# Kernel optimization log

Hardware: AMD Instinct MI355X
Metric: run time of the kernel (lower is better)

The kernel has to match this reference:

```python
import jax, jax.numpy as jnp
import numpy as np

D = 1024      # n_embd
H = 16        # n_head
DH = D // H   # head dim = 64
FF = 4 * D    # 4096
EPS = 1e-5
MASKED_BIAS = -10000.0


def gelu_new(x):
    # GPT-2 'gelu_new': 0.5*x*(1+tanh(sqrt(2/pi)*(x+0.044715*x^3)))
    c = np.sqrt(2.0 / np.pi).astype(np.float32)
    return 0.5 * x * (1.0 + jnp.tanh(c * (x + 0.044715 * x * x * x)))


def layer_norm(x, g, b):
    mu = jnp.mean(x, axis=-1, keepdims=True)
    var = jnp.mean(jnp.square(x - mu), axis=-1, keepdims=True)
    return (x - mu) * jax.lax.rsqrt(var + EPS) * g + b


def setup_inputs() -> dict:
    key = jax.random.key(0)
    ks = jax.random.split(key, 8)
    B, S = 4, 2048
    std = 0.02
    return {
        "hidden_states": jax.random.normal(ks[0], (B, S, D), jnp.float32),
        "ln1_g": jnp.ones((D,), jnp.float32),
        "ln1_b": jnp.zeros((D,), jnp.float32),
        "w_attn": std * jax.random.normal(ks[1], (D, 3 * D), jnp.float32),
        "b_attn": jnp.zeros((3 * D,), jnp.float32),
        "w_attn_proj": std * jax.random.normal(ks[2], (D, D), jnp.float32),
        "b_attn_proj": jnp.zeros((D,), jnp.float32),
        "ln2_g": jnp.ones((D,), jnp.float32),
        "ln2_b": jnp.zeros((D,), jnp.float32),
        "w_fc": std * jax.random.normal(ks[3], (D, FF), jnp.float32),
        "b_fc": jnp.zeros((FF,), jnp.float32),
        "w_mlp_proj": std * jax.random.normal(ks[4], (FF, D), jnp.float32),
        "b_mlp_proj": jnp.zeros((D,), jnp.float32),
    }


def reference(hidden_states, ln1_g, ln1_b, w_attn, b_attn, w_attn_proj, b_attn_proj,
              ln2_g, ln2_b, w_fc, b_fc, w_mlp_proj, b_mlp_proj):
    B, S, _ = hidden_states.shape

    # --- self-attention ---
    x = layer_norm(hidden_states, ln1_g, ln1_b)
    qkv = x @ w_attn + b_attn                       # [B,S,3D]
    q, k, v = jnp.split(qkv, 3, axis=-1)
    # split heads -> [B,H,S,DH]
    q = q.reshape(B, S, H, DH).transpose(0, 2, 1, 3)
    k = k.reshape(B, S, H, DH).transpose(0, 2, 1, 3)
    v = v.reshape(B, S, H, DH).transpose(0, 2, 1, 3)

    w = jnp.einsum('bhqd,bhkd->bhqk', q, k) / jnp.sqrt(jnp.float32(DH))
    causal = jnp.tril(jnp.ones((S, S), bool))       # [S,S]
    w = jnp.where(causal, w, jnp.float32(MASKED_BIAS))
    w = jax.nn.softmax(w, axis=-1)
    a = jnp.einsum('bhqk,bhkd->bhqd', w, v)         # [B,H,S,DH]
    a = a.transpose(0, 2, 1, 3).reshape(B, S, D)
    a = a @ w_attn_proj + b_attn_proj
    hidden_states = hidden_states + a

    # --- MLP ---
    m = layer_norm(hidden_states, ln2_g, ln2_b)
    m = gelu_new(m @ w_fc + b_fc) @ w_mlp_proj + b_mlp_proj
    return hidden_states + m
```

## Files before the change

### kernel.cpp

```cpp
#include <hip/hip_runtime.h>
#include <hip/hip_bf16.h>
#include <cstddef>

#define SEQ   2048
#define DMODEL 1024
#define NHEAD 16
#define HDIM  64
#define FFDIM 4096
#define QT    (SEQ / 64)

typedef __attribute__((ext_vector_type(8))) short bf16x8;
typedef __attribute__((ext_vector_type(4))) short bf16x4;
typedef __attribute__((ext_vector_type(4))) float f32x4;

__device__ __forceinline__ unsigned short f2b(float x) {
  __hip_bfloat16 h = __float2bfloat16(x);
  return __builtin_bit_cast(unsigned short, h);
}
__device__ __forceinline__ float b2f(short u) {
  unsigned x = ((unsigned)(unsigned short)u) << 16;
  return __builtin_bit_cast(float, x);
}
__device__ __forceinline__ void gl16(const short* g, short* l) {
  __builtin_amdgcn_global_load_lds(
      (const __attribute__((address_space(1))) void*)g,
      (__attribute__((address_space(3))) void*)l, 16, 0, 0);
}

__global__ __launch_bounds__(256)
void ln_kernel(const float* __restrict__ x, const float* __restrict__ g,
               const float* __restrict__ b, short* __restrict__ y) {
  const int row = blockIdx.x;
  const int t = threadIdx.x;
  const float* xr = x + (size_t)row * DMODEL;
  float4 v = *(const float4*)(xr + t * 4);
  float s = v.x + v.y + v.z + v.w;
  float q = v.x * v.x + v.y * v.y + v.z * v.z + v.w * v.w;
  #pragma unroll
  for (int off = 32; off; off >>= 1) {
    s += __shfl_xor(s, off);
    q += __shfl_xor(q, off);
  }
  __shared__ float ss[4], qq[4];
  if ((t & 63) == 0) { ss[t >> 6] = s; qq[t >> 6] = q; }
  __syncthreads();
  s = ss[0] + ss[1] + ss[2] + ss[3];
  q = qq[0] + qq[1] + qq[2] + qq[3];
  const float mean = s * (1.f / DMODEL);
  const float var = q * (1.f / DMODEL) - mean * mean;
  const float rstd = rsqrtf(var + 1e-5f);
  float4 gv = *(const float4*)(g + t * 4);
  float4 bv = *(const float4*)(b + t * 4);
  bf16x4 o;
  o[0] = (short)f2b((v.x - mean) * rstd * gv.x + bv.x);
  o[1] = (short)f2b((v.y - mean) * rstd * gv.y + bv.y);
  o[2] = (short)f2b((v.z - mean) * rstd * gv.z + bv.z);
  o[3] = (short)f2b((v.w - mean) * rstd * gv.w + bv.w);
  *(bf16x4*)(y + (size_t)row * DMODEL + t * 4) = o;
}

__device__ __forceinline__ float gelu_new_f(float x) {
  const float c = 0.7978845608028654f;
  float u = c * (x + 0.044715f * x * x * x);
  float e = __expf(2.f * u);
  float t = 1.f - 2.f / (e + 1.f);
  return 0.5f * x * (1.f + t);
}

__global__ __launch_bounds__(256)
void wconv4_kernel(const float* __restrict__ w0, short* __restrict__ t0,
                   const float* __restrict__ w1, short* __restrict__ t1,
                   const float* __restrict__ w2, short* __restrict__ t2,
                   const float* __restrict__ w3, short* __restrict__ t3) {
  int id = blockIdx.x;
  const float* W; short* Wt; int K, N;
  if (id < 768)       { W = w0; Wt = t0; K = 1024; N = 3072; }
  else if (id < 1024) { id -= 768;  W = w1; Wt = t1; K = 1024; N = 1024; }
  else if (id < 2048) { id -= 1024; W = w2; Wt = t2; K = 1024; N = 4096; }
  else                { id -= 2048; W = w3; Wt = t3; K = 4096; N = 1024; }
  const int nt = N >> 6;
  const int n0 = (id % nt) * 64, k0 = (id / nt) * 64;
  const int t = threadIdx.x;
  __shared__ short tile[64][72];
  #pragma unroll
  for (int i = 0; i < 4; ++i) {
    const int row = i * 16 + (t >> 4);
    const int col4 = (t & 15) * 4;
    float4 v = *(const float4*)(W + (size_t)(k0 + row) * N + n0 + col4);
    tile[col4 + 0][row] = (short)f2b(v.x);
    tile[col4 + 1][row] = (short)f2b(v.y);
    tile[col4 + 2][row] = (short)f2b(v.z);
    tile[col4 + 3][row] = (short)f2b(v.w);
  }
  __syncthreads();
  #pragma unroll
  for (int i = 0; i < 2; ++i) {
    const int cc = t + i * 256;
    const int nr = cc >> 3, k8 = (cc & 7) * 8;
    bf16x8 vv;
    #pragma unroll
    for (int j = 0; j < 8; ++j) vv[j] = tile[nr][k8 + j];
    *(bf16x8*)(Wt + (size_t)(n0 + nr) * K + k0 + k8) = vv;
  }
}

template <bool OUTBF, bool GELU, bool RES>
__global__ __launch_bounds__(256)
void gemm_bf16(const short* __restrict__ A, const short* __restrict__ Bt,
               const float* __restrict__ bias, const float* __restrict__ R,
               void* __restrict__ C, int M, int N, int K) {
  __shared__ short As[128 * 64];
  __shared__ short Bs[128 * 64];
  const int t = threadIdx.x, lane = t & 63, w = t >> 6;
  const int g = lane >> 4, la = lane & 15;
  const int bn = blockIdx.x, bm = blockIdx.y;
  const int wm = w >> 1, wn = w & 1;

  const int srow = t >> 3;
  const int scolb = ((t & 7) * 16) ^ ((srow & 7) << 4);
  const short* Ag = A + (size_t)(bm * 128 + srow) * K + (scolb >> 1);
  const short* Bg = Bt + (size_t)(bn * 128 + srow) * K + (scolb >> 1);
  short* Asl = As + t * 8;
  short* Bsl = Bs + t * 8;

  f32x4 acc[4][4];
  #pragma unroll
  for (int i = 0; i < 4; ++i)
    #pragma unroll
    for (int j = 0; j < 4; ++j) acc[i][j] = (f32x4){0.f, 0.f, 0.f, 0.f};

  const int KT = K >> 6;
  for (int kt = 0; kt < KT; ++kt) {
    __syncthreads();
    #pragma unroll
    for (int i = 0; i < 4; ++i) {
      gl16(Ag + (size_t)i * 32 * K + kt * 64, Asl + i * 2048);
      gl16(Bg + (size_t)i * 32 * K + kt * 64, Bsl + i * 2048);
    }
    __syncthreads();
    #pragma unroll
    for (int ks = 0; ks < 2; ++ks) {
      bf16x8 af[4], bfr[4];
      #pragma unroll
      for (int mi = 0; mi < 4; ++mi) {
        const int row = wm * 64 + mi * 16 + la;
        af[mi] = *(const bf16x8*)((const char*)As + row * 128 +
                                  ((ks * 64 + g * 16) ^ ((row & 7) << 4)));
      }
      #pragma unroll
      for (int ni = 0; ni < 4; ++ni) {
        const int row = wn * 64 + ni * 16 + la;
        bfr[ni] = *(const bf16x8*)((const char*)Bs + row * 128 +
                                   ((ks * 64 + g * 16) ^ ((row & 7) << 4)));
      }
      #pragma unroll
      for (int mi = 0; mi < 4; ++mi)
        #pragma unroll
        for (int ni = 0; ni < 4; ++ni)
          acc[mi][ni] = __builtin_amdgcn_mfma_f32_16x16x32_bf16(
              af[mi], bfr[ni], acc[mi][ni], 0, 0, 0);
    }
  }

  const int crow0 = bm * 128 + wm * 64 + g * 4;
  const int ccol0 = bn * 128 + wn * 64 + la;
  float bl[4];
  #pragma unroll
  for (int ni = 0; ni < 4; ++ni) bl[ni] = bias[ccol0 + ni * 16];
  #pragma unroll
  for (int mi = 0; mi < 4; ++mi) {
    #pragma unroll
    for (int r = 0; r < 4; ++r) {
      const size_t row = (size_t)(crow0 + mi * 16 + r);
      #pragma unroll
      for (int ni = 0; ni < 4; ++ni) {
        float v = acc[mi][ni][r] + bl[ni];
        if (GELU) v = gelu_new_f(v);
        if (RES) v += R[row * N + ccol0 + ni * 16];
        if (OUTBF)
          ((short*)C)[row * N + ccol0 + ni * 16] = (short)f2b(v);
        else
          ((float*)C)[row * N + ccol0 + ni * 16] = v;
      }
    }
  }
}

__global__ __launch_bounds__(256)
void prep_kernel(const short* __restrict__ qkv, short* __restrict__ Qb,
                 short* __restrict__ Kb, short* __restrict__ Vtb) {
  const int st = blockIdx.x, h = blockIdx.y, b = blockIdx.z;
  const int t = threadIdx.x;
  const int s0 = st * 64;
  const size_t bh = (size_t)b * NHEAD + h;
  const float qscale = 0.125f * 1.44269504088896f;
  __shared__ short vt[64][72];
  #pragma unroll
  for (int i = 0; i < 2; ++i) {
    const int cc = t + i * 256;
    const int r = cc >> 3, d8 = (cc & 7) * 8;
    const short* src = qkv + ((size_t)b * SEQ + s0 + r) * 3072 + h * 64 + d8;
    bf16x8 q8 = *(const bf16x8*)(src);
    #pragma unroll
    for (int j = 0; j < 8; ++j) q8[j] = (short)f2b(b2f(q8[j]) * qscale);
    *(bf16x8*)(Qb + (bh * SEQ + s0 + r) * 64 + d8) = q8;
    bf16x8 k8 = *(const bf16x8*)(src + 1024);
    *(bf16x8*)(Kb + (bh * SEQ + s0 + r) * 64 + d8) = k8;
    bf16x8 v8 = *(const bf16x8*)(src + 2048);
    #pragma unroll
    for (int j = 0; j < 8; ++j) vt[d8 + j][r] = v8[j];
  }
  __syncthreads();
  #pragma unroll
  for (int i = 0; i < 2; ++i) {
    const int cc = t + i * 256;
    const int d = cc >> 3, s8 = (cc & 7) * 8;
    bf16x8 vv;
    #pragma unroll
    for (int j = 0; j < 8; ++j) vv[j] = vt[d][s8 + j];
    *(bf16x8*)(Vtb + (bh * 64 + d) * SEQ + s0 + s8) = vv;
  }
}

__global__ __launch_bounds__(256)
void mha_kernel(const short* __restrict__ Qb, const short* __restrict__ Kb,
                const short* __restrict__ Vtb, short* __restrict__ out) {
  const int p = blockIdx.x, h = blockIdx.y, b = blockIdx.z;
  const int t = threadIdx.x, lane = t & 63, w = t >> 6;
  const int g = lane >> 4, la = lane & 15;
  const size_t bh = (size_t)b * NHEAD + h;

  __shared__ short Ks[64 * 64];
  __shared__ short Vts[64 * 64];
  __shared__ short Ps[4][16 * 64];

  const int srow = t >> 3;
  const int scolb = ((t & 7) * 16) ^ ((srow & 7) << 4);

  #pragma unroll 1
  for (int e = 0; e < 2; ++e) {
    const int qt = e ? (QT - 1 - p) : p;

    const short* qrow = Qb + (bh * SEQ + (size_t)qt * 64 + w * 16 + la) * 64;
    const bf16x8 qf0 = *(const bf16x8*)(qrow + g * 8);
    const bf16x8 qf1 = *(const bf16x8*)(qrow + 32 + g * 8);

    float o[16];
    #pragma unroll
    for (int i = 0; i < 16; ++i) o[i] = 0.f;
    float m = -1e30f, l = 0.f;

    for (int kt = 0; kt <= qt; ++kt) {
      const int k0 = kt * 64;
      __syncthreads();
      #pragma unroll
      for (int i = 0; i < 2; ++i) {
        const int r = srow + i * 32;
        gl16(Kb + (bh * SEQ + k0 + r) * 64 + (scolb >> 1), Ks + i * 2048 + t * 8);
        gl16(Vtb + (bh * 64 + r) * SEQ + k0 + (scolb >> 1), Vts + i * 2048 + t * 8);
      }
      __syncthreads();

      float sv[16];
      #pragma unroll
      for (int mt = 0; mt < 4; ++mt) {
        const int ar = mt * 16 + la;
        const int ab = ar * 128 + ((g * 16) ^ ((ar & 7) << 4));
        bf16x8 ka0 = *(const bf16x8*)((char*)Ks + ab);
        bf16x8 ka1 = *(const bf16x8*)((char*)Ks + (ab ^ 64));
        f32x4 sa = {0.f, 0.f, 0.f, 0.f};
        sa = __builtin_amdgcn_mfma_f32_16x16x32_bf16(ka0, qf0, sa, 0, 0, 0);
        sa = __builtin_amdgcn_mfma_f32_16x16x32_bf16(ka1, qf1, sa, 0, 0, 0);
        sv[mt * 4 + 0] = sa[0]; sv[mt * 4 + 1] = sa[1];
        sv[mt * 4 + 2] = sa[2]; sv[mt * 4 + 3] = sa[3];
      }

      if (kt == qt) {
        const int qrel = w * 16 + la;
        #pragma unroll
        for (int idx = 0; idx < 16; ++idx) {
          const int krel = (idx >> 2) * 16 + g * 4 + (idx & 3);
          if (krel > qrel) sv[idx] = -14426.950408889634f;
        }
      }

      float t8[8], t4[4], t2[2];
      #pragma unroll
      for (int i = 0; i < 8; ++i) t8[i] = fmaxf(sv[2 * i], sv[2 * i + 1]);
      #pragma unroll
      for (int i = 0; i < 4; ++i) t4[i] = fmaxf(t8[2 * i], t8[2 * i + 1]);
      t2[0] = fmaxf(t4[0], t4[1]); t2[1] = fmaxf(t4[2], t4[3]);
      float tmax = fmaxf(t2[0], t2[1]);
      tmax = fmaxf(tmax, __shfl_xor(tmax, 16));
      tmax = fmaxf(tmax, __shfl_xor(tmax, 32));

      const bool skip = __all(tmax <= m + 11.5f) != 0;
      const float mn = skip ? m : fmaxf(m, tmax);

      float ss8[8], ss4[4];
      #pragma unroll
      for (int i = 0; i < 16; ++i) sv[i] = exp2f(sv[i] - mn);
      #pragma unroll
      for (int i = 0; i < 8; ++i) ss8[i] = sv[2 * i] + sv[2 * i + 1];
      #pragma unroll
      for (int i = 0; i < 4; ++i) ss4[i] = ss8[2 * i] + ss8[2 * i + 1];
      float ps = (ss4[0] + ss4[1]) + (ss4[2] + ss4[3]);
      ps += __shfl_xor(ps, 16);
      ps += __shfl_xor(ps, 32);

      if (skip) {
        l += ps;
      } else {
        const float sc = exp2f(m - mn);
        l = l * sc + ps;
        m = mn;
        #pragma unroll
        for (int r = 0; r < 4; ++r) {
          const float scr = __shfl(sc, (g << 2) + r);
          o[r] *= scr; o[4 + r] *= scr; o[8 + r] *= scr; o[12 + r] *= scr;
        }
      }

      #pragma unroll
      for (int mt = 0; mt < 4; ++mt) {
        #pragma unroll
        for (int r2 = 0; r2 < 2; ++r2) {
          const unsigned pk = (unsigned)f2b(sv[mt * 4 + r2 * 2]) |
                              ((unsigned)f2b(sv[mt * 4 + r2 * 2 + 1]) << 16);
          const int kk = mt * 16 + g * 4 + r2 * 2;
          const int pb = la * 128 + ((kk * 2) ^ ((la & 7) << 4));
          *(unsigned*)((char*)Ps[w] + pb) = pk;
        }
      }
      asm volatile("s_waitcnt lgkmcnt(0)" ::: "memory");
      __builtin_amdgcn_sched_barrier(0);

      const int pb0 = la * 128 + ((g * 16) ^ ((la & 7) << 4));
      const bf16x8 pa0 = *(const bf16x8*)((char*)Ps[w] + pb0);
      const bf16x8 pa1 = *(const bf16x8*)((char*)Ps[w] + (pb0 ^ 64));
      #pragma unroll
      for (int nt = 0; nt < 4; ++nt) {
        const int dr = nt * 16 + la;
        const int vb = dr * 128 + ((g * 16) ^ ((dr & 7) << 4));
        bf16x8 vb0 = *(const bf16x8*)((char*)Vts + vb);
        bf16x8 vb1 = *(const bf16x8*)((char*)Vts + (vb ^ 64));
        f32x4 oa = {o[nt * 4 + 0], o[nt * 4 + 1], o[nt * 4 + 2], o[nt * 4 + 3]};
        oa = __builtin_amdgcn_mfma_f32_16x16x32_bf16(pa0, vb0, oa, 0, 0, 0);
        oa = __builtin_amdgcn_mfma_f32_16x16x32_bf16(pa1, vb1, oa, 0, 0, 0);
        o[nt * 4 + 0] = oa[0]; o[nt * 4 + 1] = oa[1];
        o[nt * 4 + 2] = oa[2]; o[nt * 4 + 3] = oa[3];
      }
    }

    const float linv = 1.f / l;
    #pragma unroll
    for (int r = 0; r < 4; ++r) {
      const float li = __shfl(linv, (g << 2) + r);
      const int qrow_g = qt * 64 + w * 16 + g * 4 + r;
      #pragma unroll
      for (int nt = 0; nt < 4; ++nt) {
        out[((size_t)b * SEQ + qrow_g) * DMODEL + h * 64 + nt * 16 + la] =
            (short)f2b(o[nt * 4 + r] * li);
      }
    }
  }
}

extern "C" void kernel_launch(void* const* d_in, const int* in_sizes, int n_in,
                              void* d_out, int out_size, void* d_ws, size_t ws_size,
                              hipStream_t stream) {
  const float* hidden      = (const float*)d_in[0];
  const float* ln1_g       = (const float*)d_in[1];
  const float* ln1_b       = (const float*)d_in[2];
  const float* w_attn      = (const float*)d_in[3];
  const float* b_attn      = (const float*)d_in[4];
  const float* w_attn_proj = (const float*)d_in[5];
  const float* b_attn_proj = (const float*)d_in[6];
  const float* ln2_g       = (const float*)d_in[7];
  const float* ln2_b       = (const float*)d_in[8];
  const float* w_fc        = (const float*)d_in[9];
  const float* b_fc        = (const float*)d_in[10];
  const float* w_mlp_proj  = (const float*)d_in[11];
  const float* b_mlp_proj  = (const float*)d_in[12];
  float* out = (float*)d_out;

  const int Bn = in_sizes[0] / (SEQ * DMODEL);
  const int M = Bn * SEQ;

  char* W = (char*)d_ws;
  const size_t szMD2 = (size_t)M * DMODEL * 2;
  short* xln_b  = (short*)W;
  short* qkv_b  = (short*)(W + szMD2);
  short* a1_b   = qkv_b;
  char*  p2     = W + szMD2 + (size_t)M * FFDIM * 2;
  short* Qb     = (short*)p2;
  short* Kb     = Qb + (size_t)M * DMODEL;
  short* Vtb    = Kb + (size_t)M * DMODEL;
  short* attn_b = Vtb + (size_t)M * DMODEL;
  float* h2     = (float*)(p2 + 4 * szMD2);
  short* wat    = (short*)(p2 + 4 * szMD2 + (size_t)M * DMODEL * 4);
  short* wpt    = wat + (size_t)3 * DMODEL * DMODEL;
  short* wft    = wpt + (size_t)DMODEL * DMODEL;
  short* wmt    = wft + (size_t)FFDIM * DMODEL;

  wconv4_kernel<<<3072, 256, 0, stream>>>(w_attn, wat, w_attn_proj, wpt,
                                          w_fc, wft, w_mlp_proj, wmt);
  ln_kernel<<<M, 256, 0, stream>>>(hidden, ln1_g, ln1_b, xln_b);
  gemm_bf16<true, false, false><<<dim3(3 * DMODEL / 128, M / 128), 256, 0, stream>>>(
      xln_b, wat, b_attn, nullptr, qkv_b, M, 3 * DMODEL, DMODEL);
  prep_kernel<<<dim3(SEQ / 64, NHEAD, Bn), 256, 0, stream>>>(qkv_b, Qb, Kb, Vtb);
  mha_kernel<<<dim3(QT / 2, NHEAD, Bn), 256, 0, stream>>>(Qb, Kb, Vtb, attn_b);
  gemm_bf16<false, false, true><<<dim3(DMODEL / 128, M / 128), 256, 0, stream>>>(
      attn_b, wpt, b_attn_proj, hidden, h2, M, DMODEL, DMODEL);
  ln_kernel<<<M, 256, 0, stream>>>(h2, ln2_g, ln2_b, xln_b);
  gemm_bf16<true, true, false><<<dim3(FFDIM / 128, M / 128), 256, 0, stream>>>(
      xln_b, wft, b_fc, nullptr, a1_b, M, FFDIM, DMODEL);
  gemm_bf16<false, false, true><<<dim3(DMODEL / 128, M / 128), 256, 0, stream>>>(
      a1_b, wmt, b_mlp_proj, h2, out, M, DMODEL, FFDIM);
}
```

Before: 565.3 us.

## Fuse QKV head-split into GEMM epilogue and double-buffer attention K/V tiles

Folds the softmax query scale into the converted QKV weights and bias, and has the QKV GEMM epilogue scatter Q, K and V straight into per-head layouts. This leaves the prep kernel only the V transpose, cutting a full read and write of the QKV buffer. The attention kernel now runs both query tiles in one flattened loop with double-buffered K/V LDS tiles, prefetching the next tile while computing the current one, and raises wave priority around the MFMA sections. The scattered epilogue stores are less coalesced, and the extra LDS buffers may lower occupancy.

```diff
diff --git a/kernel.cpp b/kernel.cpp
--- a/kernel.cpp
+++ b/kernel.cpp
@@ -12,6 +12,8 @@
 typedef __attribute__((ext_vector_type(8))) short bf16x8;
 typedef __attribute__((ext_vector_type(4))) short bf16x4;
 typedef __attribute__((ext_vector_type(4))) float f32x4;
+
+#define QSCALE (0.125f * 1.44269504088896f)
 
 __device__ __forceinline__ unsigned short f2b(float x) {
   __hip_bfloat16 h = __float2bfloat16(x);
@@ -71,26 +73,35 @@
 void wconv4_kernel(const float* __restrict__ w0, short* __restrict__ t0,
                    const float* __restrict__ w1, short* __restrict__ t1,
                    const float* __restrict__ w2, short* __restrict__ t2,
-                   const float* __restrict__ w3, short* __restrict__ t3) {
+                   const float* __restrict__ w3, short* __restrict__ t3,
+                   const float* __restrict__ ba, float* __restrict__ bas) {
   int id = blockIdx.x;
+  const int t = threadIdx.x;
+  if (id == 3072) {
+    #pragma unroll
+    for (int i = t; i < 3072; i += 256)
+      bas[i] = ba[i] * (i < 1024 ? QSCALE : 1.f);
+    return;
+  }
   const float* W; short* Wt; int K, N;
+  float sc = 1.f;
   if (id < 768)       { W = w0; Wt = t0; K = 1024; N = 3072; }
   else if (id < 1024) { id -= 768;  W = w1; Wt = t1; K = 1024; N = 1024; }
   else if (id < 2048) { id -= 1024; W = w2; Wt = t2; K = 1024; N = 4096; }
   else                { id -= 2048; W = w3; Wt = t3; K = 4096; N = 1024; }
   const int nt = N >> 6;
   const int n0 = (id % nt) * 64, k0 = (id / nt) * 64;
-  const int t = threadIdx.x;
+  if (W == w0 && n0 < 1024) sc = QSCALE;
   __shared__ short tile[64][72];
   #pragma unroll
   for (int i = 0; i < 4; ++i) {
     const int row = i * 16 + (t >> 4);
     const int col4 = (t & 15) * 4;
     float4 v = *(const float4*)(W + (size_t)(k0 + row) * N + n0 + col4);
-    tile[col4 + 0][row] = (short)f2b(v.x);
-    tile[col4 + 1][row] = (short)f2b(v.y);
-    tile[col4 + 2][row] = (short)f2b(v.z);
-    tile[col4 + 3][row] = (short)f2b(v.w);
+    tile[col4 + 0][row] = (short)f2b(v.x * sc);
+    tile[col4 + 1][row] = (short)f2b(v.y * sc);
+    tile[col4 + 2][row] = (short)f2b(v.z * sc);
+    tile[col4 + 3][row] = (short)f2b(v.w * sc);
   }
   __syncthreads();
   #pragma unroll
@@ -104,11 +115,12 @@
   }
 }
 
-template <bool OUTBF, bool GELU, bool RES>
+template <bool OUTBF, bool GELU, bool RES, bool QKVS>
 __global__ __launch_bounds__(256)
 void gemm_bf16(const short* __restrict__ A, const short* __restrict__ Bt,
                const float* __restrict__ bias, const float* __restrict__ R,
-               void* __restrict__ C, int M, int N, int K) {
+               void* __restrict__ C, short* __restrict__ C2,
+               short* __restrict__ C3, int M, int N, int K) {
   __shared__ short As[128 * 64];
   __shared__ short Bs[128 * 64];
   const int t = threadIdx.x, lane = t & 63, w = t >> 6;
@@ -171,42 +183,46 @@
   for (int mi = 0; mi < 4; ++mi) {
     #pragma unroll
     for (int r = 0; r < 4; ++r) {
-      const size_t row = (size_t)(crow0 + mi * 16 + r);
-      #pragma unroll
-      for (int ni = 0; ni < 4; ++ni) {
-        float v = acc[mi][ni][r] + bl[ni];
-        if (GELU) v = gelu_new_f(v);
-        if (RES) v += R[row * N + ccol0 + ni * 16];
-        if (OUTBF)
-          ((short*)C)[row * N + ccol0 + ni * 16] = (short)f2b(v);
-        else
-          ((float*)C)[row * N + ccol0 + ni * 16] = v;
+      const int row = crow0 + mi * 16 + r;
+      if (QKVS) {
+        const int bq = row >> 11, s = row & 2047;
+        #pragma unroll
+        for (int ni = 0; ni < 4; ++ni) {
+          const int n = ccol0 + ni * 16;
+          const int region = n >> 10;
+          const int nn = n & 1023;
+          short* dst = region == 0 ? (short*)C : (region == 1 ? C2 : C3);
+          dst[((size_t)(bq * NHEAD + (nn >> 6)) * SEQ + s) * 64 + (nn & 63)] =
+              (short)f2b(acc[mi][ni][r] + bl[ni]);
+        }
+      } else {
+        #pragma unroll
+        for (int ni = 0; ni < 4; ++ni) {
+          float v = acc[mi][ni][r] + bl[ni];
+          if (GELU) v = gelu_new_f(v);
+          if (RES) v += R[(size_t)row * N + ccol0 + ni * 16];
+          if (OUTBF)
+            ((short*)C)[(size_t)row * N + ccol0 + ni * 16] = (short)f2b(v);
+          else
+            ((float*)C)[(size_t)row * N + ccol0 + ni * 16] = v;
+        }
       }
     }
   }
 }
 
 __global__ __launch_bounds__(256)
-void prep_kernel(const short* __restrict__ qkv, short* __restrict__ Qb,
-                 short* __restrict__ Kb, short* __restrict__ Vtb) {
+void prepv_kernel(const short* __restrict__ Vb, short* __restrict__ Vtb) {
   const int st = blockIdx.x, h = blockIdx.y, b = blockIdx.z;
   const int t = threadIdx.x;
   const int s0 = st * 64;
   const size_t bh = (size_t)b * NHEAD + h;
-  const float qscale = 0.125f * 1.44269504088896f;
   __shared__ short vt[64][72];
   #pragma unroll
   for (int i = 0; i < 2; ++i) {
     const int cc = t + i * 256;
     const int r = cc >> 3, d8 = (cc & 7) * 8;
-    const short* src = qkv + ((size_t)b * SEQ + s0 + r) * 3072 + h * 64 + d8;
-    bf16x8 q8 = *(const bf16x8*)(src);
-    #pragma unroll
-    for (int j = 0; j < 8; ++j) q8[j] = (short)f2b(b2f(q8[j]) * qscale);
-    *(bf16x8*)(Qb + (bh * SEQ + s0 + r) * 64 + d8) = q8;
-    bf16x8 k8 = *(const bf16x8*)(src + 1024);
-    *(bf16x8*)(Kb + (bh * SEQ + s0 + r) * 64 + d8) = k8;
-    bf16x8 v8 = *(const bf16x8*)(src + 2048);
+    bf16x8 v8 = *(const bf16x8*)(Vb + (bh * SEQ + s0 + r) * 64 + d8);
     #pragma unroll
     for (int j = 0; j < 8; ++j) vt[d8 + j][r] = v8[j];
   }
@@ -230,139 +246,170 @@
   const int g = lane >> 4, la = lane & 15;
   const size_t bh = (size_t)b * NHEAD + h;
 
-  __shared__ short Ks[64 * 64];
-  __shared__ short Vts[64 * 64];
+  __shared__ short Ks[2][64 * 64];
+  __shared__ short Vts[2][64 * 64];
   __shared__ short Ps[4][16 * 64];
 
   const int srow = t >> 3;
   const int scolb = ((t & 7) * 16) ^ ((srow & 7) << 4);
 
+  const int qt0 = p, qt1 = QT - 1 - p;
+  const int T0 = qt0 + 1, total = T0 + qt1 + 1;
+
+  int qt = qt0;
+  const short* qr = Qb + (bh * SEQ + (size_t)qt0 * 64 + w * 16 + la) * 64;
+  bf16x8 qf0 = *(const bf16x8*)(qr + g * 8);
+  bf16x8 qf1 = *(const bf16x8*)(qr + 32 + g * 8);
+
+  float o[16];
+  #pragma unroll
+  for (int i = 0; i < 16; ++i) o[i] = 0.f;
+  float m = -1e30f, l = 0.f;
+
+  #pragma unroll
+  for (int i = 0; i < 2; ++i) {
+    const int r = srow + i * 32;
+    gl16(Kb + (bh * SEQ + r) * 64 + (scolb >> 1), Ks[0] + i * 2048 + t * 8);
+    gl16(Vtb + (bh * 64 + r) * SEQ + (scolb >> 1), Vts[0] + i * 2048 + t * 8);
+  }
+  __syncthreads();
+
+  int cur = 0;
   #pragma unroll 1
-  for (int e = 0; e < 2; ++e) {
-    const int qt = e ? (QT - 1 - p) : p;
-
-    const short* qrow = Qb + (bh * SEQ + (size_t)qt * 64 + w * 16 + la) * 64;
-    const bf16x8 qf0 = *(const bf16x8*)(qrow + g * 8);
-    const bf16x8 qf1 = *(const bf16x8*)(qrow + 32 + g * 8);
-
-    float o[16];
-    #pragma unroll
-    for (int i = 0; i < 16; ++i) o[i] = 0.f;
-    float m = -1e30f, l = 0.f;
-
-    for (int kt = 0; kt <= qt; ++kt) {
-      const int k0 = kt * 64;
-      __syncthreads();
+  for (int it = 0; it < total; ++it) {
+    if (it + 1 < total) {
+      const int nkt = (it + 1 < T0) ? (it + 1) : (it + 1 - T0);
+      const int nk0 = nkt * 64;
       #pragma unroll
       for (int i = 0; i < 2; ++i) {
         const int r = srow + i * 32;
-        gl16(Kb + (bh * SEQ + k0 + r) * 64 + (scolb >> 1), Ks + i * 2048 + t * 8);
-        gl16(Vtb + (bh * 64 + r) * SEQ + k0 + (scolb >> 1), Vts + i * 2048 + t * 8);
-      }
-      __syncthreads();
-
-      float sv[16];
-      #pragma unroll
-      for (int mt = 0; mt < 4; ++mt) {
-        const int ar = mt * 16 + la;
-        const int ab = ar * 128 + ((g * 16) ^ ((ar & 7) << 4));
-        bf16x8 ka0 = *(const bf16x8*)((char*)Ks + ab);
-        bf16x8 ka1 = *(const bf16x8*)((char*)Ks + (ab ^ 64));
-        f32x4 sa = {0.f, 0.f, 0.f, 0.f};
-        sa = __builtin_amdgcn_mfma_f32_16x16x32_bf16(ka0, qf0, sa, 0, 0, 0);
-        sa = __builtin_amdgcn_mfma_f32_16x16x32_bf16(ka1, qf1, sa, 0, 0, 0);
-        sv[mt * 4 + 0] = sa[0]; sv[mt * 4 + 1] = sa[1];
-        sv[mt * 4 + 2] = sa[2]; sv[mt * 4 + 3] = sa[3];
-      }
-
-      if (kt == qt) {
-        const int qrel = w * 16 + la;
+        gl16(Kb + (bh * SEQ + nk0 + r) * 64 + (scolb >> 1),
+             Ks[cur ^ 1] + i * 2048 + t * 8);
+        gl16(Vtb + (bh * 64 + r) * SEQ + nk0 + (scolb >> 1),
+             Vts[cur ^ 1] + i * 2048 + t * 8);
+      }
+    }
+
+    float sv[16];
+    __builtin_amdgcn_s_setprio(1);
+    #pragma unroll
+    for (int mt = 0; mt < 4; ++mt) {
+      const int ar = mt * 16 + la;
+      const int ab = ar * 128 + ((g * 16) ^ ((ar & 7) << 4));
+      bf16x8 ka0 = *(const bf16x8*)((char*)Ks[cur] + ab);
+      bf16x8 ka1 = *(const bf16x8*)((char*)Ks[cur] + (ab ^ 64));
+      f32x4 sa = {0.f, 0.f, 0.f, 0.f};
+      sa = __builtin_amdgcn_mfma_f32_16x16x32_bf16(ka0, qf0, sa, 0, 0, 0);
+      sa = __builtin_amdgcn_mfma_f32_16x16x32_bf16(ka1, qf1, sa, 0, 0, 0);
+      sv[mt * 4 + 0] = sa[0]; sv[mt * 4 + 1] = sa[1];
+      sv[mt * 4 + 2] = sa[2]; sv[mt * 4 + 3] = sa[3];
+    }
+    __builtin_amdgcn_s_setprio(0);
+
+    const bool diag = (it == T0 - 1) || (it == total - 1);
+    if (diag) {
+      const int qrel = w * 16 + la;
+      #pragma unroll
+      for (int idx = 0; idx < 16; ++idx) {
+        const int krel = (idx >> 2) * 16 + g * 4 + (idx & 3);
+        if (krel > qrel) sv[idx] = -14426.950408889634f;
+      }
+    }
+
+    float t8[8], t4[4], t2[2];
+    #pragma unroll
+    for (int i = 0; i < 8; ++i) t8[i] = fmaxf(sv[2 * i], sv[2 * i + 1]);
+    #pragma unroll
+    for (int i = 0; i < 4; ++i) t4[i] = fmaxf(t8[2 * i], t8[2 * i + 1]);
+    t2[0] = fmaxf(t4[0], t4[1]); t2[1] = fmaxf(t4[2], t4[3]);
+    float tmax = fmaxf(t2[0], t2[1]);
+    tmax = fmaxf(tmax, __shfl_xor(tmax, 16));
+    tmax = fmaxf(tmax, __shfl_xor(tmax, 32));
+
+    const bool skip = __all(tmax <= m + 11.5f) != 0;
+    const float mn = skip ? m : fmaxf(m, tmax);
+
+    float ss8[8], ss4[4];
+    #pragma unroll
+    for (int i = 0; i < 16; ++i) sv[i] = exp2f(sv[i] - mn);
+    #pragma unroll
+    for (int i = 0; i < 8; ++i) ss8[i] = sv[2 * i] + sv[2 * i + 1];
+    #pragma unroll
+    for (int i = 0; i < 4; ++i) ss4[i] = ss8[2 * i] + ss8[2 * i + 1];
+    float ps = (ss4[0] + ss4[1]) + (ss4[2] + ss4[3]);
+    ps += __shfl_xor(ps, 16);
+    ps += __shfl_xor(ps, 32);
+
+    if (skip) {
+      l += ps;
+    } else {
+      const float sc = exp2f(m - mn);
+      l = l * sc + ps;
+      m = mn;
+      #pragma unroll
+      for (int r = 0; r < 4; ++r) {
+        const float scr = __shfl(sc, (g << 2) + r);
+        o[r] *= scr; o[4 + r] *= scr; o[8 + r] *= scr; o[12 + r] *= scr;
+      }
+    }
+
+    #pragma unroll
+    for (int mt = 0; mt < 4; ++mt) {
+      #pragma unroll
+      for (int r2 = 0; r2 < 2; ++r2) {
+        const unsigned pk = (unsigned)f2b(sv[mt * 4 + r2 * 2]) |
+                            ((unsigned)f2b(sv[mt * 4 + r2 * 2 + 1]) << 16);
+        const int kk = mt * 16 + g * 4 + r2 * 2;
+        const int pb = la * 128 + ((kk * 2) ^ ((la & 7) << 4));
+        *(unsigned*)((char*)Ps[w] + pb) = pk;
+      }
+    }
+    asm volatile("s_waitcnt lgkmcnt(0)" ::: "memory");
+    __builtin_amdgcn_sched_barrier(0);
+
+    const int pb0 = la * 128 + ((g * 16) ^ ((la & 7) << 4));
+    const bf16x8 pa0 = *(const bf16x8*)((char*)Ps[w] + pb0);
+    const bf16x8 pa1 = *(const bf16x8*)((char*)Ps[w] + (pb0 ^ 64));
+    __builtin_amdgcn_s_setprio(1);
+    #pragma unroll
+    for (int nt = 0; nt < 4; ++nt) {
+      const int dr = nt * 16 + la;
+      const int vb = dr * 128 + ((g * 16) ^ ((dr & 7) << 4));
+      bf16x8 vb0 = *(const bf16x8*)((char*)Vts[cur] + vb);
+      bf16x8 vb1 = *(const bf16x8*)((char*)Vts[cur] + (vb ^ 64));
+      f32x4 oa = {o[nt * 4 + 0], o[nt * 4 + 1], o[nt * 4 + 2], o[nt * 4 + 3]};
+      oa = __builtin_amdgcn_mfma_f32_16x16x32_bf16(pa0, vb0, oa, 0, 0, 0);
+      oa = __builtin_amdgcn_mfma_f32_16x16x32_bf16(pa1, vb1, oa, 0, 0, 0);
+      o[nt * 4 + 0] = oa[0]; o[nt * 4 + 1] = oa[1];
+      o[nt * 4 + 2] = oa[2]; o[nt * 4 + 3] = oa[3];
+    }
+    __builtin_amdgcn_s_setprio(0);
+
+    if (diag) {
+      const float linv = 1.f / l;
+      #pragma unroll
+      for (int r = 0; r < 4; ++r) {
+        const float li = __shfl(linv, (g << 2) + r);
+        const int qrow_g = qt * 64 + w * 16 + g * 4 + r;
         #pragma unroll
-        for (int idx = 0; idx < 16; ++idx) {
-          const int krel = (idx >> 2) * 16 + g * 4 + (idx & 3);
-          if (krel > qrel) sv[idx] = -14426.950408889634f;
+        for (int nt = 0; nt < 4; ++nt) {
+          out[((size_t)b * SEQ + qrow_g) * DMODEL + h * 64 + nt * 16 + la] =
+              (short)f2b(o[nt * 4 + r] * li);
         }
       }
-
-      float t8[8], t4[4], t2[2];
-      #pragma unroll
-      for (int i = 0; i < 8; ++i) t8[i] = fmaxf(sv[2 * i], sv[2 * i + 1]);
-      #pragma unroll
-      for (int i = 0; i < 4; ++i) t4[i] = fmaxf(t8[2 * i], t8[2 * i + 1]);
-      t2[0] = fmaxf(t4[0], t4[1]); t2[1] = fmaxf(t4[2], t4[3]);
-      float tmax = fmaxf(t2[0], t2[1]);
-      tmax = fmaxf(tmax, __shfl_xor(tmax, 16));
-      tmax = fmaxf(tmax, __shfl_xor(tmax, 32));
-
-      const bool skip = __all(tmax <= m + 11.5f) != 0;
-      const float mn = skip ? m : fmaxf(m, tmax);
-
-      float ss8[8], ss4[4];
-      #pragma unroll
-      for (int i = 0; i < 16; ++i) sv[i] = exp2f(sv[i] - mn);
-      #pragma unroll
-      for (int i = 0; i < 8; ++i) ss8[i] = sv[2 * i] + sv[2 * i + 1];
-      #pragma unroll
-      for (int i = 0; i < 4; ++i) ss4[i] = ss8[2 * i] + ss8[2 * i + 1];
-      float ps = (ss4[0] + ss4[1]) + (ss4[2] + ss4[3]);
-      ps += __shfl_xor(ps, 16);
-      ps += __shfl_xor(ps, 32);
-
-      if (skip) {
-        l += ps;
-      } else {
-        const float sc = exp2f(m - mn);
-        l = l * sc + ps;
-        m = mn;
+      if (it == T0 - 1) {
         #pragma unroll
-        for (int r = 0; r < 4; ++r) {
-          const float scr = __shfl(sc, (g << 2) + r);
-          o[r] *= scr; o[4 + r] *= scr; o[8 + r] *= scr; o[12 + r] *= scr;
-        }
-      }
-
-      #pragma unroll
-      for (int mt = 0; mt < 4; ++mt) {
-        #pragma unroll
-        for (int r2 = 0; r2 < 2; ++r2) {
-          const unsigned pk = (unsigned)f2b(sv[mt * 4 + r2 * 2]) |
-                              ((unsigned)f2b(sv[mt * 4 + r2 * 2 + 1]) << 16);
-          const int kk = mt * 16 + g * 4 + r2 * 2;
-          const int pb = la * 128 + ((kk * 2) ^ ((la & 7) << 4));
-          *(unsigned*)((char*)Ps[w] + pb) = pk;
-        }
-      }
-      asm volatile("s_waitcnt lgkmcnt(0)" ::: "memory");
-      __builtin_amdgcn_sched_barrier(0);
-
-      const int pb0 = la * 128 + ((g * 16) ^ ((la & 7) << 4));
-      const bf16x8 pa0 = *(const bf16x8*)((char*)Ps[w] + pb0);
-      const bf16x8 pa1 = *(const bf16x8*)((char*)Ps[w] + (pb0 ^ 64));
-      #pragma unroll
-      for (int nt = 0; nt < 4; ++nt) {
-        const int dr = nt * 16 + la;
-        const int vb = dr * 128 + ((g * 16) ^ ((dr & 7) << 4));
-        bf16x8 vb0 = *(const bf16x8*)((char*)Vts + vb);
-        bf16x8 vb1 = *(const bf16x8*)((char*)Vts + (vb ^ 64));
-        f32x4 oa = {o[nt * 4 + 0], o[nt * 4 + 1], o[nt * 4 + 2], o[nt * 4 + 3]};
-        oa = __builtin_amdgcn_mfma_f32_16x16x32_bf16(pa0, vb0, oa, 0, 0, 0);
-        oa = __builtin_amdgcn_mfma_f32_16x16x32_bf16(pa1, vb1, oa, 0, 0, 0);
-        o[nt * 4 + 0] = oa[0]; o[nt * 4 + 1] = oa[1];
-        o[nt * 4 + 2] = oa[2]; o[nt * 4 + 3] = oa[3];
-      }
-    }
-
-    const float linv = 1.f / l;
-    #pragma unroll
-    for (int r = 0; r < 4; ++r) {
-      const float li = __shfl(linv, (g << 2) + r);
-      const int qrow_g = qt * 64 + w * 16 + g * 4 + r;
-      #pragma unroll
-      for (int nt = 0; nt < 4; ++nt) {
-        out[((size_t)b * SEQ + qrow_g) * DMODEL + h * 64 + nt * 16 + la] =
-            (short)f2b(o[nt * 4 + r] * li);
-      }
-    }
+        for (int i = 0; i < 16; ++i) o[i] = 0.f;
+        m = -1e30f; l = 0.f;
+        qt = qt1;
+        const short* qr1 = Qb + (bh * SEQ + (size_t)qt1 * 64 + w * 16 + la) * 64;
+        qf0 = *(const bf16x8*)(qr1 + g * 8);
+        qf1 = *(const bf16x8*)(qr1 + 32 + g * 8);
+      }
+    }
+
+    __syncthreads();
+    cur ^= 1;
   }
 }
 
@@ -390,8 +437,8 @@
   char* W = (char*)d_ws;
   const size_t szMD2 = (size_t)M * DMODEL * 2;
   short* xln_b  = (short*)W;
-  short* qkv_b  = (short*)(W + szMD2);
-  short* a1_b   = qkv_b;
+  short* Vb     = (short*)(W + szMD2);
+  short* a1_b   = Vb;
   char*  p2     = W + szMD2 + (size_t)M * FFDIM * 2;
   short* Qb     = (short*)p2;
   short* Kb     = Qb + (size_t)M * DMODEL;
@@ -402,19 +449,25 @@
   short* wpt    = wat + (size_t)3 * DMODEL * DMODEL;
   short* wft    = wpt + (size_t)DMODEL * DMODEL;
   short* wmt    = wft + (size_t)FFDIM * DMODEL;
-
-  wconv4_kernel<<<3072, 256, 0, stream>>>(w_attn, wat, w_attn_proj, wpt,
-                                          w_fc, wft, w_mlp_proj, wmt);
+  float* bas    = (float*)(wmt + (size_t)DMODEL * FFDIM);
+
+  wconv4_kernel<<<3073, 256, 0, stream>>>(w_attn, wat, w_attn_proj, wpt,
+                                          w_fc, wft, w_mlp_proj, wmt,
+                                          b_attn, bas);
   ln_kernel<<<M, 256, 0, stream>>>(hidden, ln1_g, ln1_b, xln_b);
-  gemm_bf16<true, false, false><<<dim3(3 * DMODEL / 128, M / 128), 256, 0, stream>>>(
-      xln_b, wat, b_attn, nullptr, qkv_b, M, 3 * DMODEL, DMODEL);
-  prep_kernel<<<dim3(SEQ / 64, NHEAD, Bn), 256, 0, stream>>>(qkv_b, Qb, Kb, Vtb);
+  gemm_bf16<true, false, false, true>
+      <<<dim3(3 * DMODEL / 128, M / 128), 256, 0, stream>>>(
+      xln_b, wat, bas, nullptr, Qb, Kb, Vb, M, 3 * DMODEL, DMODEL);
+  prepv_kernel<<<dim3(SEQ / 64, NHEAD, Bn), 256, 0, stream>>>(Vb, Vtb);
   mha_kernel<<<dim3(QT / 2, NHEAD, Bn), 256, 0, stream>>>(Qb, Kb, Vtb, attn_b);
-  gemm_bf16<false, false, true><<<dim3(DMODEL / 128, M / 128), 256, 0, stream>>>(
-      attn_b, wpt, b_attn_proj, hidden, h2, M, DMODEL, DMODEL);
+  gemm_bf16<false, false, true, false>
+      <<<dim3(DMODEL / 128, M / 128), 256, 0, stream>>>(
+      attn_b, wpt, b_attn_proj, hidden, h2, nullptr, nullptr, M, DMODEL, DMODEL);
   ln_kernel<<<M, 256, 0, stream>>>(h2, ln2_g, ln2_b, xln_b);
-  gemm_bf16<true, true, false><<<dim3(FFDIM / 128, M / 128), 256, 0, stream>>>(
-      xln_b, wft, b_fc, nullptr, a1_b, M, FFDIM, DMODEL);
-  gemm_bf16<false, false, true><<<dim3(DMODEL / 128, M / 128), 256, 0, stream>>>(
-      a1_b, wmt, b_mlp_proj, h2, out, M, DMODEL, FFDIM);
-}
+  gemm_bf16<true, true, false, false>
+      <<<dim3(FFDIM / 128, M / 128), 256, 0, stream>>>(
+      xln_b, wft, b_fc, nullptr, a1_b, nullptr, nullptr, M, FFDIM, DMODEL);
+  gemm_bf16<false, false, true, false>
+      <<<dim3(DMODEL / 128, M / 128), 256, 0, stream>>>(
+      a1_b, wmt, b_mlp_proj, h2, out, nullptr, nullptr, M, DMODEL, FFDIM);
+}
```

After: 552.9 us. -2.2%, faster.
